# Kernel optimization log

Measured on AMD Instinct MI355X. Metric: run time of the kernel, lower is better.

The kernel has to match this reference:

```python
import jax, jax.numpy as jnp
import numpy as np

D_MODEL = 256
D_INNER = 512    # expand=2
D_STATE = 16
D_CONV = 4
DT_RANK = 16     # ceil(256/16)
N_BLOCKS = 4
EPS = 1e-5


def setup_inputs() -> dict:
    key = jax.random.key(0)
    ks = jax.random.split(key, 8)
    s = 0.02
    return {
        "x": jax.random.normal(ks[0], (1, 4, D_MODEL, 32, 32), jnp.float32),
        "norm_w": jnp.ones((N_BLOCKS, D_MODEL), jnp.float32),
        "norm_b": jnp.zeros((N_BLOCKS, D_MODEL), jnp.float32),
        "in_w": jax.random.normal(ks[1], (N_BLOCKS, 2 * D_INNER, D_MODEL), jnp.float32) * s,
        "conv_w": jax.random.normal(ks[2], (N_BLOCKS, D_INNER, D_CONV), jnp.float32) * s,
        "conv_b": jnp.zeros((N_BLOCKS, D_INNER), jnp.float32),
        "xproj_w": jax.random.normal(ks[3], (N_BLOCKS, DT_RANK + 2 * D_STATE, D_INNER), jnp.float32) * s,
        "dtproj_w": jax.random.normal(ks[4], (N_BLOCKS, D_INNER, DT_RANK), jnp.float32) * s,
        "dtproj_b": jax.random.normal(ks[5], (N_BLOCKS, D_INNER), jnp.float32) * s,
        "A_log": jnp.tile(jnp.log(jnp.arange(1, D_STATE + 1, dtype=jnp.float32))[None, None, :],
                          (N_BLOCKS, D_INNER, 1)),
        "Dp": jnp.ones((N_BLOCKS, D_INNER), jnp.float32),
        "out_w": jax.random.normal(ks[6], (N_BLOCKS, D_MODEL, D_INNER), jnp.float32) * s,
    }


def _layernorm(x, w, b):
    mu = jnp.mean(x, axis=-1, keepdims=True)
    var = jnp.var(x, axis=-1, keepdims=True)
    return (x - mu) / jnp.sqrt(var + EPS) * w + b


def _mamba(h, in_w, conv_w, conv_b, xproj_w, dtproj_w, dtproj_b, A_log, Dp, out_w):
    # h: (B, L, d_model)
    B, L, _ = h.shape
    xz = h @ in_w.T                                   # (B, L, 2*d_inner)
    x, z = jnp.split(xz, 2, axis=-1)
    # causal depthwise conv1d, kernel size D_CONV
    xp = jnp.pad(x, ((0, 0), (D_CONV - 1, 0), (0, 0)))
    xc = sum(xp[:, k:k + L, :] * conv_w[:, k] for k in range(D_CONV)) + conv_b
    x = jax.nn.silu(xc)                               # (B, L, d_inner)
    dbl = x @ xproj_w.T                               # (B, L, dt_rank + 2*d_state)
    dt = dbl[..., :DT_RANK]
    Bm = dbl[..., DT_RANK:DT_RANK + D_STATE]          # (B, L, n)
    Cm = dbl[..., DT_RANK + D_STATE:]                 # (B, L, n)
    dt = jax.nn.softplus(dt @ dtproj_w.T + dtproj_b)  # (B, L, d_inner)
    A = -jnp.exp(A_log)                               # (d_inner, n)
    dA = jnp.exp(dt[..., None] * A)                   # (B, L, d_inner, n)
    dBx = dt[..., None] * Bm[:, :, None, :] * x[..., None]

    def step(hprev, inp):
        dA_t, dBx_t, C_t = inp
        hcur = dA_t * hprev + dBx_t                   # (B, d_inner, n)
        return hcur, jnp.einsum('bdn,bn->bd', hcur, C_t)

    h0 = jnp.zeros((B, D_INNER, D_STATE), x.dtype)
    _, y = jax.lax.scan(step, h0, (dA.transpose(1, 0, 2, 3),
                                   dBx.transpose(1, 0, 2, 3),
                                   Cm.transpose(1, 0, 2)))
    y = y.transpose(1, 0, 2)                          # (B, L, d_inner)
    y = (y + Dp * x) * jax.nn.silu(z)
    return y @ out_w.T                                # (B, L, d_model)


def _forward(x, norm_w, norm_b, in_w, conv_w, conv_b, xproj_w, dtproj_w, dtproj_b, A_log, Dp, out_w):
    b, n, c, h, w = x.shape
    hs = x.reshape(b * n, c, h * w).transpose(0, 2, 1)  # (bn, hw, c)

    def blk(i, hidden, resid):
        resid = hidden if resid is None else resid + hidden
        hn = _layernorm(resid, norm_w[i], norm_b[i])
        out = _mamba(hn, in_w[i], conv_w[i], conv_b[i], xproj_w[i],
                     dtproj_w[i], dtproj_b[i], A_log[i], Dp[i], out_w[i])
        return out, resid

    res = None
    for i in range(2):  # pairs of (forward, backward-flipped) blocks
        hf, rf = blk(2 * i, hs, res)
        hb, rb = blk(2 * i + 1, hs[:, ::-1], None if res is None else res[:, ::-1])
        hs = hf + hb[:, ::-1]
        res = rf + rb[:, ::-1]
    res = res + hs
    return res.transpose(0, 2, 1).reshape(b, n, c, h, w)


def reference(x, norm_w, norm_b, in_w, conv_w, conv_b, xproj_w, dtproj_w, dtproj_b, A_log, Dp, out_w):
    return _forward(x, norm_w, norm_b, in_w, conv_w, conv_b, xproj_w,
                    dtproj_w, dtproj_b, A_log, Dp, out_w)
```

## Files before the change

### kernel.cpp

```cpp
#include <hip/hip_runtime.h>
#include <math.h>


__device__ __forceinline__ float sigmoidf_(float x){ return 1.f/(1.f+__expf(-x)); }
__device__ __forceinline__ short bf16_(float x){
  unsigned u = __float_as_uint(x);
  u += 0x7FFFu + ((u>>16)&1u);
  return (short)(u>>16);
}

using fragAB = __attribute__((ext_vector_type(8))) short;
using fragC  = __attribute__((ext_vector_type(4))) float;

__global__ __launch_bounds__(256) void k_transpose_in(const float* __restrict__ x, float* __restrict__ hs){
  __shared__ float tile[32][33];
  int b = blockIdx.z;
  int l0 = blockIdx.x*32, c0 = blockIdx.y*32;
  int tx = threadIdx.x, ty = threadIdx.y;
  #pragma unroll
  for (int j=0;j<32;j+=8)
    tile[ty+j][tx] = x[(size_t)b*262144 + (size_t)(c0+ty+j)*1024 + l0 + tx];
  __syncthreads();
  #pragma unroll
  for (int j=0;j<32;j+=8)
    hs[(size_t)b*262144 + (size_t)(l0+ty+j)*256 + (c0+tx)] = tile[tx][ty+j];
}

__global__ __launch_bounds__(256) void k_final(const float* __restrict__ racc, const float* __restrict__ hs, float* __restrict__ out){
  __shared__ float tile[32][33];
  int b = blockIdx.z;
  int l0 = blockIdx.x*32, c0 = blockIdx.y*32;
  int tx = threadIdx.x, ty = threadIdx.y;
  #pragma unroll
  for (int j=0;j<32;j+=8){
    size_t idx = (size_t)b*262144 + (size_t)(l0+ty+j)*256 + c0+tx;
    tile[ty+j][tx] = 2.f*racc[idx] + hs[idx];
  }
  __syncthreads();
  #pragma unroll
  for (int j=0;j<32;j+=8)
    out[(size_t)b*262144 + (size_t)(c0+ty+j)*1024 + l0+tx] = tile[tx][ty+j];
}

__global__ __launch_bounds__(256) void k_ln(const float* __restrict__ hs, float* __restrict__ racc, short* __restrict__ hn_f,
  const float* __restrict__ nw, const float* __restrict__ nb, int layer0, int first){
  int row = blockIdx.x, c = threadIdx.x;
  size_t idx = (size_t)row*256 + c;
  float r = hs[idx];
  if (!first) r += 2.f*racc[idx];
  racc[idx] = r;
  float s1=r, s2=r*r;
  #pragma unroll
  for (int o=32;o>=1;o>>=1){ s1+=__shfl_xor(s1,o); s2+=__shfl_xor(s2,o); }
  __shared__ float red[8];
  int wid=c>>6, lane=c&63;
  if (lane==0){ red[wid]=s1; red[4+wid]=s2; }
  __syncthreads();
  s1 = red[0]+red[1]+red[2]+red[3];
  s2 = red[4]+red[5]+red[6]+red[7];
  float mu = s1*(1.f/256.f);
  float var = s2*(1.f/256.f) - mu*mu;
  float inv = rsqrtf(var + 1e-5f);
  float nv = (r-mu)*inv;
  size_t fo = (((size_t)(row>>4)*32 + (c>>3))*16 + (row&15))*8 + (c&7);
  hn_f[fo]           = bf16_(nv*nw[layer0*256+c] + nb[layer0*256+c]);
  hn_f[1048576 + fo] = bf16_(nv*nw[(layer0+1)*256+c] + nb[(layer0+1)*256+c]);
}

__global__ __launch_bounds__(256) void k_wconv(
  const float* __restrict__ inw, const float* __restrict__ xpw,
  const float* __restrict__ dtw, const float* __restrict__ otw,
  short* __restrict__ f_inw, short* __restrict__ f_xpw,
  short* __restrict__ f_dtw, short* __restrict__ f_otw,
  short* __restrict__ dt_f)
{
  int which = blockIdx.y, layer = blockIdx.z;
  int idx = blockIdx.x*256 + threadIdx.x;
  if (which==4){
    if (layer) return;
    if (idx >= 131072) return;
    int st = idx >> 16, rem = idx & 65535;
    int mt = rem >> 8, kt2 = (rem>>7)&1, e = rem&127;
    dt_f[(size_t)st*131072 + ((size_t)(mt*4 + 2 + kt2))*128 + e] = 0;
    return;
  }
  const float* src; short* dst; int R,K,Kp;
  if (which==0){ src=inw; dst=f_inw; R=1024; K=256; Kp=256; }
  else if (which==1){ src=xpw; dst=f_xpw; R=48; K=512; Kp=512; }
  else if (which==2){ src=dtw; dst=f_dtw; R=512; K=16; Kp=32; }
  else { src=otw; dst=f_otw; R=256; K=512; Kp=512; }
  int per = (R>>4)*(Kp>>3)*128;
  if (idx >= per) return;
  int e = idx & 127, tile = idx >> 7;
  int nkt = Kp>>3;
  int kt = tile % nkt, rt = tile / nkt;
  int r = rt*16 + (e>>3), k = kt*8 + (e&7);
  float v = (k<K) ? src[((size_t)layer*R + r)*K + k] : 0.f;
  dst[(size_t)layer*per + idx] = bf16_(v);
}

__global__ __launch_bounds__(256) void k_mm(
  const short* __restrict__ Af, long sA,
  const short* __restrict__ Wf, long sW,
  const short* __restrict__ A2f, const short* __restrict__ W2f,
  float* __restrict__ Cb, long sC,
  const float* __restrict__ biasb, long sBias,
  int M, int N, int K, int ldc, int mode,
  short* __restrict__ dtf, long sDtf)
{
  int z = blockIdx.z;
  int tid = threadIdx.x;
  int lane = tid & 63, wid = tid >> 6;
  int wm = wid & 1, wn = wid >> 1;
  int K8 = K >> 3;
  int mt_base = blockIdx.y*8 + wm*4;
  int nt_base = blockIdx.x*4 + wn*2;
  int ncap = (N + 15) >> 4;
  const int loff = lane*8;
  fragC acc[4][2] = {};
  const short* Aps[2] = { Af + (size_t)z*sA, A2f };
  const short* Wps[2] = { Wf + (size_t)z*sW, W2f };
  int nseg = A2f ? 2 : 1;
  for (int sgi=0; sgi<nseg; ++sgi){
    const short* A = Aps[sgi];
    const short* W = Wps[sgi];
    for (int kt=0; kt<K8; kt+=4){
      fragAB a[4], b[2];
      #pragma unroll
      for (int i=0;i<4;++i)
        a[i] = *(const fragAB*)(A + ((size_t)(mt_base+i)*K8 + kt)*128 + loff);
      #pragma unroll
      for (int j=0;j<2;++j){
        int nt = nt_base + j; if (nt >= ncap) nt = ncap-1;
        b[j] = *(const fragAB*)(W + ((size_t)nt*K8 + kt)*128 + loff);
      }
      #pragma unroll
      for (int i=0;i<4;++i)
        #pragma unroll
        for (int j=0;j<2;++j)
          acc[i][j] = __builtin_amdgcn_mfma_f32_16x16x32_bf16(a[i], b[j], acc[i][j], 0,0,0);
    }
  }
  float* C = Cb + (size_t)z*sC;
  const float* bias = biasb ? biasb + (size_t)z*sBias : nullptr;
  int r0 = (lane>>4)*4;
  int cc = lane & 15;
  #pragma unroll
  for (int i=0;i<4;++i){
    int row = (mt_base+i)*16 + r0;
    #pragma unroll
    for (int j=0;j<2;++j){
      int col = (nt_base+j)*16 + cc;
      if (col < N){
        #pragma unroll
        for (int r=0;r<4;++r){
          float v = acc[i][j][r];
          if (bias) v += bias[col];
          if (mode==2){ v = (v > 20.f) ? v : log1pf(__expf(v)); }
          C[(size_t)(row+r)*ldc + col] = v;
          if (mode==1 && col < 16){
            int rr = row + r;
            dtf[(size_t)z*sDtf + (((size_t)(rr>>4)*4 + (col>>3))*16 + (rr&15))*8 + (col&7)] = bf16_(v);
          }
        }
      }
    }
  }
}

__global__ __launch_bounds__(256) void k_conv(const float* __restrict__ xz, float* __restrict__ xc,
  short* __restrict__ xc_f, const float* __restrict__ cw, const float* __restrict__ cb, int layer0){
  int idx = blockIdx.x*256 + threadIdx.x;
  int d = idx & 511;
  int t = (idx >> 9) & 1023;
  int sb = idx >> 19;
  int s = sb >> 2, b = sb & 3;
  int layer = layer0 + s;
  const float* w = cw + ((size_t)layer*512 + d)*4;
  float accv = cb[(size_t)layer*512 + d];
  const float* xp = xz + (size_t)sb*1048576;
  if (s==0){
    #pragma unroll
    for (int k=0;k<4;++k){ int tt = t + k - 3; if (tt>=0) accv = fmaf(xp[(size_t)tt*1024 + d], w[k], accv); }
  } else {
    #pragma unroll
    for (int k=0;k<4;++k){ int tt = t + 3 - k; if (tt<1024) accv = fmaf(xp[(size_t)tt*1024 + d], w[k], accv); }
  }
  float v = accv * sigmoidf_(accv);
  xc[idx] = v;
  int row = b*1024 + t;
  xc_f[(size_t)s*2097152 + (((size_t)(row>>4)*64 + (d>>3))*16 + (row&15))*8 + (d&7)] = bf16_(v);
}

#define NCHUNK 32
#define CSTEPS 32

__global__ __launch_bounds__(256) void k_scan_a(
  const float* __restrict__ dtv, const float* __restrict__ xc,
  const float* __restrict__ dbl, const float* __restrict__ A_log,
  float* __restrict__ dtsum, float* __restrict__ hF, int layer0)
{
  int d = blockIdx.x*256 + threadIdx.x;
  int k = blockIdx.y;
  int sb = blockIdx.z;
  int s = sb >> 2;
  int layer = layer0 + s;
  float Av[16];
  #pragma unroll
  for (int n=0;n<16;++n) Av[n] = -__expf(A_log[((size_t)layer*512 + d)*16 + n]);
  const float* dt_p = dtv + (size_t)sb*524288 + d;
  const float* xc_p = xc + (size_t)sb*524288 + d;
  const float* bc_p = dbl + (size_t)sb*49152;
  float h[16];
  #pragma unroll
  for (int n=0;n<16;++n) h[n] = 0.f;
  float ssum = 0.f;
  int u0 = k*CSTEPS;
  for (int i=0;i<CSTEPS;++i){
    int u = u0 + i;
    int t = s ? (1023 - u) : u;
    float dtval = dt_p[(size_t)t*512];
    float xv = xc_p[(size_t)t*512];
    const float4* bp = (const float4*)(bc_p + (size_t)t*48 + 16);
    float4 B0 = bp[0], B1 = bp[1], B2 = bp[2], B3 = bp[3];
    float Bv[16] = {B0.x,B0.y,B0.z,B0.w,B1.x,B1.y,B1.z,B1.w,
                    B2.x,B2.y,B2.z,B2.w,B3.x,B3.y,B3.z,B3.w};
    float w = dtval * xv;
    ssum += dtval;
    #pragma unroll
    for (int n=0;n<16;++n)
      h[n] = fmaf(__expf(dtval*Av[n]), h[n], w*Bv[n]);
  }
  size_t base = (size_t)(sb*NCHUNK + k)*512 + d;
  dtsum[base] = ssum;
  float4* hp = (float4*)(hF + base*16);
  #pragma unroll
  for (int q=0;q<4;++q) hp[q] = make_float4(h[4*q],h[4*q+1],h[4*q+2],h[4*q+3]);
}

__global__ __launch_bounds__(256) void k_scan_c(
  const float* __restrict__ dtsum, float* __restrict__ hF,
  const float* __restrict__ A_log, int layer0)
{
  int gid = blockIdx.x*256 + threadIdx.x;
  int sb = gid >> 13;
  int d = (gid >> 4) & 511;
  int n = gid & 15;
  int layer = layer0 + (sb >> 2);
  float Av = -__expf(A_log[((size_t)layer*512 + d)*16 + n]);
  float hrun = 0.f;
  #pragma unroll
  for (int k=0;k<NCHUNK;++k){
    size_t base = (size_t)(sb*NCHUNK + k)*512 + d;
    float a = __expf(Av * dtsum[base]);
    float hf = hF[base*16 + n];
    hF[base*16 + n] = hrun;
    hrun = fmaf(a, hrun, hf);
  }
}

__global__ __launch_bounds__(256) void k_scan_b(
  const float* __restrict__ dtv, const float* __restrict__ xc, const float* __restrict__ xz,
  const float* __restrict__ dbl, const float* __restrict__ A_log, const float* __restrict__ Dp,
  const float* __restrict__ h0p, short* __restrict__ y_f, int layer0)
{
  int d = blockIdx.x*256 + threadIdx.x;
  int k = blockIdx.y;
  int sb = blockIdx.z;
  int s = sb >> 2, b = sb & 3;
  int layer = layer0 + s;
  float Av[16];
  #pragma unroll
  for (int n=0;n<16;++n) Av[n] = -__expf(A_log[((size_t)layer*512 + d)*16 + n]);
  float Dv = Dp[(size_t)layer*512 + d];
  const float* dt_p = dtv + (size_t)sb*524288 + d;
  const float* xc_p = xc + (size_t)sb*524288 + d;
  const float* z_p = xz + (size_t)sb*1048576 + 512 + d;
  const float* bc_p = dbl + (size_t)sb*49152;
  size_t base = (size_t)(sb*NCHUNK + k)*512 + d;
  float h[16];
  const float4* hp = (const float4*)(h0p + base*16);
  #pragma unroll
  for (int q=0;q<4;++q){
    float4 v = hp[q];
    h[4*q]=v.x; h[4*q+1]=v.y; h[4*q+2]=v.z; h[4*q+3]=v.w;
  }
  short* yo = y_f + (size_t)s*2097152;
  int u0 = k*CSTEPS;
  for (int i=0;i<CSTEPS;++i){
    int u = u0 + i;
    int t = s ? (1023 - u) : u;
    float dtval = dt_p[(size_t)t*512];
    float xv = xc_p[(size_t)t*512];
    const float4* bp = (const float4*)(bc_p + (size_t)t*48 + 16);
    float4 B0 = bp[0], B1 = bp[1], B2 = bp[2], B3 = bp[3];
    float4 C0 = bp[4], C1 = bp[5], C2 = bp[6], C3 = bp[7];
    float Bv[16] = {B0.x,B0.y,B0.z,B0.w,B1.x,B1.y,B1.z,B1.w,
                    B2.x,B2.y,B2.z,B2.w,B3.x,B3.y,B3.z,B3.w};
    float Cv[16] = {C0.x,C0.y,C0.z,C0.w,C1.x,C1.y,C1.z,C1.w,
                    C2.x,C2.y,C2.z,C2.w,C3.x,C3.y,C3.z,C3.w};
    float w = dtval * xv;
    float y = 0.f;
    #pragma unroll
    for (int n=0;n<16;++n){
      h[n] = fmaf(__expf(dtval*Av[n]), h[n], w*Bv[n]);
      y = fmaf(h[n], Cv[n], y);
    }
    float zv = z_p[(size_t)t*1024];
    float yv = (y + Dv*xv) * (zv*sigmoidf_(zv));
    int row = b*1024 + t;
    yo[(((size_t)(row>>4)*64 + (d>>3))*16 + (row&15))*8 + (d&7)] = bf16_(yv);
  }
}

extern "C" void kernel_launch(void* const* d_in, const int* in_sizes, int n_in,
                              void* d_out, int out_size, void* d_ws, size_t ws_size,
                              hipStream_t stream) {
  const float* x        = (const float*)d_in[0];
  const float* norm_w   = (const float*)d_in[1];
  const float* norm_b   = (const float*)d_in[2];
  const float* in_w     = (const float*)d_in[3];
  const float* conv_w   = (const float*)d_in[4];
  const float* conv_b   = (const float*)d_in[5];
  const float* xproj_w  = (const float*)d_in[6];
  const float* dtproj_w = (const float*)d_in[7];
  const float* dtproj_b = (const float*)d_in[8];
  const float* A_log    = (const float*)d_in[9];
  const float* Dp       = (const float*)d_in[10];
  const float* out_w    = (const float*)d_in[11];
  float* out = (float*)d_out;
  float* ws = (float*)d_ws;

  float* hs    = ws;
  float* racc  = ws + 1048576;
  float* hF    = ws + 2097152;
  short* hn_f  = (short*)(ws + 2097152);
  float* xz    = ws + 4194304;
  float* xc    = ws + 12582912;
  float* dbl   = ws + 16777216;
  float* dtv   = ws + 17170432;
  short* xc_f  = (short*)(ws + 21364736);
  short* y_f   = xc_f;
  short* dt_f  = (short*)(ws + 23461888);
  short* w_inw = (short*)(ws + 23592960);
  short* w_xp  = w_inw + 1048576;
  short* w_dt  = w_xp + 98304;
  short* w_out = w_dt + 65536;
  float* dtsum = hs;

  k_wconv<<<dim3(1024,5,4), 256, 0, stream>>>(in_w, xproj_w, dtproj_w, out_w,
      w_inw, w_xp, w_dt, w_out, dt_f);
  k_transpose_in<<<dim3(32,8,4), dim3(32,8), 0, stream>>>(x, hs);

  for (int it=0; it<2; ++it){
    int layer0 = 2*it;
    k_ln<<<4096, 256, 0, stream>>>(hs, racc, hn_f, norm_w, norm_b, layer0, it==0 ? 1 : 0);
    k_mm<<<dim3(16,32,2), 256, 0, stream>>>(hn_f, 1048576L, w_inw + (size_t)layer0*262144, 262144L,
        nullptr, nullptr, xz, 4194304L, nullptr, 0L, 4096, 1024, 256, 1024, 0, nullptr, 0L);
    k_conv<<<16384, 256, 0, stream>>>(xz, xc, xc_f, conv_w, conv_b, layer0);
    k_mm<<<dim3(1,32,2), 256, 0, stream>>>(xc_f, 2097152L, w_xp + (size_t)layer0*24576, 24576L,
        nullptr, nullptr, dbl, 196608L, nullptr, 0L, 4096, 48, 512, 48, 1, dt_f, 131072L);
    k_mm<<<dim3(8,32,2), 256, 0, stream>>>(dt_f, 131072L, w_dt + (size_t)layer0*16384, 16384L,
        nullptr, nullptr, dtv, 2097152L, dtproj_b + (size_t)layer0*512, 512L, 4096, 512, 32, 512, 2, nullptr, 0L);
    k_scan_a<<<dim3(2,NCHUNK,8), 256, 0, stream>>>(dtv, xc, dbl, A_log, dtsum, hF, layer0);
    k_scan_c<<<256, 256, 0, stream>>>(dtsum, hF, A_log, layer0);
    k_scan_b<<<dim3(2,NCHUNK,8), 256, 0, stream>>>(dtv, xc, xz, dbl, A_log, Dp, hF, y_f, layer0);
    k_mm<<<dim3(4,32,1), 256, 0, stream>>>(y_f, 0L, w_out + (size_t)layer0*131072, 0L,
        y_f + 2097152, w_out + (size_t)(layer0+1)*131072, hs, 0L, nullptr, 0L,
        4096, 256, 512, 256, 0, nullptr, 0L);
  }
  k_final<<<dim3(32,8,4), dim3(32,8), 0, stream>>>(racc, hs, out);
}
```

Measured before the change: 443.2 us.

## Store in_proj outputs as bf16 split x/z buffers and rechunk scan

The in_proj GEMM now writes x and z halves as separate bf16 row-major buffers instead of a fp32 interleaved xz. Conv reads bf16 and no longer writes an fp32 xc copy, and the scans read x from the bf16 fragment layout and z from the bf16 buffer. The intent is to cut global memory traffic between stages. The scan is also split into 64 chunks of 16 steps with unrolled inner loops to add parallelism, and the workspace is re-laid out. Storing x and z in bf16 lowers the precision of the scan inputs and gating.

Result: slower. 458.2 us (+3.4%).

```diff
diff --git a/kernel.cpp b/kernel.cpp
--- a/kernel.cpp
+++ b/kernel.cpp
@@ -7,6 +7,9 @@
   unsigned u = __float_as_uint(x);
   u += 0x7FFFu + ((u>>16)&1u);
   return (short)(u>>16);
+}
+__device__ __forceinline__ float f32_(short s){
+  return __uint_as_float(((unsigned)(unsigned short)s)<<16);
 }
 
 using fragAB = __attribute__((ext_vector_type(8))) short;
@@ -106,7 +109,8 @@
   float* __restrict__ Cb, long sC,
   const float* __restrict__ biasb, long sBias,
   int M, int N, int K, int ldc, int mode,
-  short* __restrict__ dtf, long sDtf)
+  short* __restrict__ aux1, long sAux1,
+  short* __restrict__ aux2, long sAux2)
 {
   int z = blockIdx.z;
   int tid = threadIdx.x;
@@ -141,7 +145,7 @@
           acc[i][j] = __builtin_amdgcn_mfma_f32_16x16x32_bf16(a[i], b[j], acc[i][j], 0,0,0);
     }
   }
-  float* C = Cb + (size_t)z*sC;
+  float* C = Cb ? Cb + (size_t)z*sC : nullptr;
   const float* bias = biasb ? biasb + (size_t)z*sBias : nullptr;
   int r0 = (lane>>4)*4;
   int cc = lane & 15;
@@ -157,10 +161,14 @@
           float v = acc[i][j][r];
           if (bias) v += bias[col];
           if (mode==2){ v = (v > 20.f) ? v : log1pf(__expf(v)); }
-          C[(size_t)(row+r)*ldc + col] = v;
-          if (mode==1 && col < 16){
-            int rr = row + r;
-            dtf[(size_t)z*sDtf + (((size_t)(rr>>4)*4 + (col>>3))*16 + (rr&15))*8 + (col&7)] = bf16_(v);
+          int rr = row + r;
+          if (mode==3){
+            if (col < 512) aux1[(size_t)z*sAux1 + (size_t)rr*512 + col] = bf16_(v);
+            else           aux2[(size_t)z*sAux2 + (size_t)rr*512 + (col-512)] = bf16_(v);
+          } else {
+            C[(size_t)rr*ldc + col] = v;
+            if (mode==1 && col < 16)
+              aux1[(size_t)z*sAux1 + (((size_t)(rr>>4)*4 + (col>>3))*16 + (rr&15))*8 + (col&7)] = bf16_(v);
           }
         }
       }
@@ -168,8 +176,8 @@
   }
 }
 
-__global__ __launch_bounds__(256) void k_conv(const float* __restrict__ xz, float* __restrict__ xc,
-  short* __restrict__ xc_f, const float* __restrict__ cw, const float* __restrict__ cb, int layer0){
+__global__ __launch_bounds__(256) void k_conv(const short* __restrict__ xb, short* __restrict__ xc_f,
+  const float* __restrict__ cw, const float* __restrict__ cb, int layer0){
   int idx = blockIdx.x*256 + threadIdx.x;
   int d = idx & 511;
   int t = (idx >> 9) & 1023;
@@ -178,49 +186,54 @@
   int layer = layer0 + s;
   const float* w = cw + ((size_t)layer*512 + d)*4;
   float accv = cb[(size_t)layer*512 + d];
-  const float* xp = xz + (size_t)sb*1048576;
+  const short* xp = xb + (size_t)s*2097152 + (size_t)b*1024*512 + d;
   if (s==0){
     #pragma unroll
-    for (int k=0;k<4;++k){ int tt = t + k - 3; if (tt>=0) accv = fmaf(xp[(size_t)tt*1024 + d], w[k], accv); }
+    for (int k=0;k<4;++k){ int tt = t + k - 3; if (tt>=0) accv = fmaf(f32_(xp[(size_t)tt*512]), w[k], accv); }
   } else {
     #pragma unroll
-    for (int k=0;k<4;++k){ int tt = t + 3 - k; if (tt<1024) accv = fmaf(xp[(size_t)tt*1024 + d], w[k], accv); }
+    for (int k=0;k<4;++k){ int tt = t + 3 - k; if (tt<1024) accv = fmaf(f32_(xp[(size_t)tt*512]), w[k], accv); }
   }
   float v = accv * sigmoidf_(accv);
-  xc[idx] = v;
   int row = b*1024 + t;
   xc_f[(size_t)s*2097152 + (((size_t)(row>>4)*64 + (d>>3))*16 + (row&15))*8 + (d&7)] = bf16_(v);
 }
 
-#define NCHUNK 32
-#define CSTEPS 32
+#define NCHUNK 64
+#define CSTEPS 16
+
+__device__ __forceinline__ float ld_xc(const short* xcf, int row, int d){
+  return f32_(xcf[(((size_t)(row>>4)*64 + (d>>3))*16 + (row&15))*8 + (d&7)]);
+}
 
 __global__ __launch_bounds__(256) void k_scan_a(
-  const float* __restrict__ dtv, const float* __restrict__ xc,
+  const float* __restrict__ dtv, const short* __restrict__ xc_f,
   const float* __restrict__ dbl, const float* __restrict__ A_log,
   float* __restrict__ dtsum, float* __restrict__ hF, int layer0)
 {
   int d = blockIdx.x*256 + threadIdx.x;
   int k = blockIdx.y;
   int sb = blockIdx.z;
-  int s = sb >> 2;
+  int s = sb >> 2, b = sb & 3;
   int layer = layer0 + s;
   float Av[16];
   #pragma unroll
   for (int n=0;n<16;++n) Av[n] = -__expf(A_log[((size_t)layer*512 + d)*16 + n]);
   const float* dt_p = dtv + (size_t)sb*524288 + d;
-  const float* xc_p = xc + (size_t)sb*524288 + d;
+  const short* xcf = xc_f + (size_t)s*2097152;
   const float* bc_p = dbl + (size_t)sb*49152;
   float h[16];
   #pragma unroll
   for (int n=0;n<16;++n) h[n] = 0.f;
   float ssum = 0.f;
   int u0 = k*CSTEPS;
+  #pragma unroll
   for (int i=0;i<CSTEPS;++i){
     int u = u0 + i;
     int t = s ? (1023 - u) : u;
+    int row = b*1024 + t;
     float dtval = dt_p[(size_t)t*512];
-    float xv = xc_p[(size_t)t*512];
+    float xv = ld_xc(xcf, row, d);
     const float4* bp = (const float4*)(bc_p + (size_t)t*48 + 16);
     float4 B0 = bp[0], B1 = bp[1], B2 = bp[2], B3 = bp[3];
     float Bv[16] = {B0.x,B0.y,B0.z,B0.w,B1.x,B1.y,B1.z,B1.w,
@@ -249,7 +262,7 @@
   int layer = layer0 + (sb >> 2);
   float Av = -__expf(A_log[((size_t)layer*512 + d)*16 + n]);
   float hrun = 0.f;
-  #pragma unroll
+  #pragma unroll 8
   for (int k=0;k<NCHUNK;++k){
     size_t base = (size_t)(sb*NCHUNK + k)*512 + d;
     float a = __expf(Av * dtsum[base]);
@@ -260,7 +273,7 @@
 }
 
 __global__ __launch_bounds__(256) void k_scan_b(
-  const float* __restrict__ dtv, const float* __restrict__ xc, const float* __restrict__ xz,
+  const float* __restrict__ dtv, const short* __restrict__ xc_f, const short* __restrict__ zb,
   const float* __restrict__ dbl, const float* __restrict__ A_log, const float* __restrict__ Dp,
   const float* __restrict__ h0p, short* __restrict__ y_f, int layer0)
 {
@@ -274,8 +287,8 @@
   for (int n=0;n<16;++n) Av[n] = -__expf(A_log[((size_t)layer*512 + d)*16 + n]);
   float Dv = Dp[(size_t)layer*512 + d];
   const float* dt_p = dtv + (size_t)sb*524288 + d;
-  const float* xc_p = xc + (size_t)sb*524288 + d;
-  const float* z_p = xz + (size_t)sb*1048576 + 512 + d;
+  const short* xcf = xc_f + (size_t)s*2097152;
+  const short* z_p = zb + (size_t)s*2097152 + (size_t)b*1024*512 + d;
   const float* bc_p = dbl + (size_t)sb*49152;
   size_t base = (size_t)(sb*NCHUNK + k)*512 + d;
   float h[16];
@@ -287,11 +300,13 @@
   }
   short* yo = y_f + (size_t)s*2097152;
   int u0 = k*CSTEPS;
+  #pragma unroll
   for (int i=0;i<CSTEPS;++i){
     int u = u0 + i;
     int t = s ? (1023 - u) : u;
+    int row = b*1024 + t;
     float dtval = dt_p[(size_t)t*512];
-    float xv = xc_p[(size_t)t*512];
+    float xv = ld_xc(xcf, row, d);
     const float4* bp = (const float4*)(bc_p + (size_t)t*48 + 16);
     float4 B0 = bp[0], B1 = bp[1], B2 = bp[2], B3 = bp[3];
     float4 C0 = bp[4], C1 = bp[5], C2 = bp[6], C3 = bp[7];
@@ -306,9 +321,8 @@
       h[n] = fmaf(__expf(dtval*Av[n]), h[n], w*Bv[n]);
       y = fmaf(h[n], Cv[n], y);
     }
-    float zv = z_p[(size_t)t*1024];
+    float zv = f32_(z_p[(size_t)t*512]);
     float yv = (y + Dv*xv) * (zv*sigmoidf_(zv));
-    int row = b*1024 + t;
     yo[(((size_t)(row>>4)*64 + (d>>3))*16 + (row&15))*8 + (d&7)] = bf16_(yv);
   }
 }
@@ -333,20 +347,20 @@
 
   float* hs    = ws;
   float* racc  = ws + 1048576;
-  float* hF    = ws + 2097152;
   short* hn_f  = (short*)(ws + 2097152);
-  float* xz    = ws + 4194304;
-  float* xc    = ws + 12582912;
-  float* dbl   = ws + 16777216;
-  float* dtv   = ws + 17170432;
-  short* xc_f  = (short*)(ws + 21364736);
-  short* y_f   = xc_f;
-  short* dt_f  = (short*)(ws + 23461888);
-  short* w_inw = (short*)(ws + 23592960);
+  short* xb    = (short*)(ws + 3145728);
+  short* zb    = (short*)(ws + 5242880);
+  short* xc_f  = (short*)(ws + 7340032);
+  short* y_f   = (short*)(ws + 9437184);
+  float* dbl   = ws + 11534336;
+  float* dtv   = ws + 12058624;
+  short* dt_f  = (short*)(ws + 16252928);
+  float* dtsum = ws + 16384000;
+  float* hF    = ws + 16646144;
+  short* w_inw = (short*)(ws + 20840448);
   short* w_xp  = w_inw + 1048576;
   short* w_dt  = w_xp + 98304;
   short* w_out = w_dt + 65536;
-  float* dtsum = hs;
 
   k_wconv<<<dim3(1024,5,4), 256, 0, stream>>>(in_w, xproj_w, dtproj_w, out_w,
       w_inw, w_xp, w_dt, w_out, dt_f);
@@ -356,18 +370,21 @@
     int layer0 = 2*it;
     k_ln<<<4096, 256, 0, stream>>>(hs, racc, hn_f, norm_w, norm_b, layer0, it==0 ? 1 : 0);
     k_mm<<<dim3(16,32,2), 256, 0, stream>>>(hn_f, 1048576L, w_inw + (size_t)layer0*262144, 262144L,
-        nullptr, nullptr, xz, 4194304L, nullptr, 0L, 4096, 1024, 256, 1024, 0, nullptr, 0L);
-    k_conv<<<16384, 256, 0, stream>>>(xz, xc, xc_f, conv_w, conv_b, layer0);
+        nullptr, nullptr, nullptr, 0L, nullptr, 0L, 4096, 1024, 256, 0, 3,
+        xb, 2097152L, zb, 2097152L);
+    k_conv<<<16384, 256, 0, stream>>>(xb, xc_f, conv_w, conv_b, layer0);
     k_mm<<<dim3(1,32,2), 256, 0, stream>>>(xc_f, 2097152L, w_xp + (size_t)layer0*24576, 24576L,
-        nullptr, nullptr, dbl, 196608L, nullptr, 0L, 4096, 48, 512, 48, 1, dt_f, 131072L);
+        nullptr, nullptr, dbl, 196608L, nullptr, 0L, 4096, 48, 512, 48, 1,
+        dt_f, 131072L, nullptr, 0L);
     k_mm<<<dim3(8,32,2), 256, 0, stream>>>(dt_f, 131072L, w_dt + (size_t)layer0*16384, 16384L,
-        nullptr, nullptr, dtv, 2097152L, dtproj_b + (size_t)layer0*512, 512L, 4096, 512, 32, 512, 2, nullptr, 0L);
-    k_scan_a<<<dim3(2,NCHUNK,8), 256, 0, stream>>>(dtv, xc, dbl, A_log, dtsum, hF, layer0);
+        nullptr, nullptr, dtv, 2097152L, dtproj_b + (size_t)layer0*512, 512L, 4096, 512, 32, 512, 2,
+        nullptr, 0L, nullptr, 0L);
+    k_scan_a<<<dim3(2,NCHUNK,8), 256, 0, stream>>>(dtv, xc_f, dbl, A_log, dtsum, hF, layer0);
     k_scan_c<<<256, 256, 0, stream>>>(dtsum, hF, A_log, layer0);
-    k_scan_b<<<dim3(2,NCHUNK,8), 256, 0, stream>>>(dtv, xc, xz, dbl, A_log, Dp, hF, y_f, layer0);
+    k_scan_b<<<dim3(2,NCHUNK,8), 256, 0, stream>>>(dtv, xc_f, zb, dbl, A_log, Dp, hF, y_f, layer0);
     k_mm<<<dim3(4,32,1), 256, 0, stream>>>(y_f, 0L, w_out + (size_t)layer0*131072, 0L,
         y_f + 2097152, w_out + (size_t)(layer0+1)*131072, hs, 0L, nullptr, 0L,
-        4096, 256, 512, 256, 0, nullptr, 0L);
+        4096, 256, 512, 256, 0, nullptr, 0L, nullptr, 0L);
   }
   k_final<<<dim3(32,8,4), dim3(32,8), 0, stream>>>(racc, hs, out);
 }
```
